# Kernel optimization log

Hardware: AMD Instinct MI355X
Metric: run time of the kernel (lower is better)

The kernel has to match this reference:

```python
import jax, jax.numpy as jnp
import numpy as np

ALPHA = 1.0  # config.cnet_alpha


def setup_inputs() -> dict:
    key = jax.random.key(0)
    k1, k2 = jax.random.split(key)
    z = jax.random.normal(k1, (8192, 2048), dtype=jnp.float32)
    centroids = jax.random.normal(k2, (512, 2048), dtype=jnp.float32)
    return {"z": z, "centroids": centroids}


def reference(z, centroids):
    # --- compute_similarity, 'EUC' branch ---
    # torch: sqrt(sum((z[None] - centroids[:, None])**2, dim=2)).T
    # computed here via the expanded quadratic form (same math, no
    # (n_clusters, bs, n_hidden) materialization):
    z_sq = jnp.sum(z * z, axis=1, keepdims=True)              # (bs, 1)
    c_sq = jnp.sum(centroids * centroids, axis=1)[None, :]    # (1, n_clusters)
    cross = jnp.einsum('bh,ch->bc', z, centroids)             # (bs, n_clusters)
    d2 = jnp.maximum(z_sq + c_sq - 2.0 * cross, 0.0)
    similarity = jnp.sqrt(d2)                                 # (bs, n_clusters)

    # --- Student-t soft assignment Q ---
    Q = jnp.power(1.0 + similarity / ALPHA, -(ALPHA + 1.0) / 2.0)
    Q = Q / jnp.nansum(Q, axis=1, keepdims=True)

    # --- target distribution P ---
    P = (Q * Q) / jnp.sum(Q, axis=0, keepdims=True)
    P = P / jnp.nansum(P, axis=1, keepdims=True)

    return jnp.stack([Q, P])  # (2, bs, n_clusters)
```

## Files before the change

### kernel.cpp

```cpp
#include <hip/hip_runtime.h>
#include <stdint.h>

#define M_ROWS 8192
#define NCLUST 512
#define KDIM   2048

#define BM 128
#define BN 128
#define BKB 128
#define KSPLIT 2
#define NKT (KDIM / KSPLIT / BKB)

typedef __attribute__((ext_vector_type(4))) int   i32x4;
typedef __attribute__((ext_vector_type(8))) int   i32x8;
typedef __attribute__((ext_vector_type(4))) float f32x4;
typedef __attribute__((ext_vector_type(8))) unsigned short u16x8;

__device__ __forceinline__ unsigned short f2bf(float f) {
    unsigned u = __float_as_uint(f);
    u += 0x7FFFu + ((u >> 16) & 1u);
    return (unsigned short)(u >> 16);
}
__device__ __forceinline__ float bf2f(unsigned short h) {
    return __uint_as_float(((unsigned)h) << 16);
}

__device__ __forceinline__ void gload_lds16(const void* g, void* l) {
    __builtin_amdgcn_global_load_lds(
        (const __attribute__((address_space(1))) void*)g,
        (__attribute__((address_space(3))) void*)l,
        16, 0, 0);
}

__global__ __launch_bounds__(256) void k_convert(
    const float* __restrict__ z, const float* __restrict__ cent,
    unsigned char* __restrict__ zb, unsigned char* __restrict__ cb,
    float* __restrict__ zsq, float* __restrict__ csq,
    float* __restrict__ colsum)
{
    int w = threadIdx.x >> 6, lane = threadIdx.x & 63;
    int row = blockIdx.x * 4 + w;

    const float* src;
    unsigned char* dst;
    float* nrm;
    int r;
    if (row < M_ROWS) { src = z + (size_t)row * KDIM; dst = zb + (size_t)row * KDIM; nrm = zsq; r = row; }
    else              { r = row - M_ROWS; src = cent + (size_t)r * KDIM; dst = cb + (size_t)r * KDIM; nrm = csq; }

    float s = 0.f;
    #pragma unroll
    for (int it = 0; it < KDIM / 256; ++it) {
        int idx = it * 256 + lane * 4;
        float4 v = *(const float4*)(src + idx);
        s += v.x * v.x + v.y * v.y + v.z * v.z + v.w * v.w;
        int p = __builtin_amdgcn_cvt_pk_fp8_f32(v.x, v.y, 0, 0);
        p     = __builtin_amdgcn_cvt_pk_fp8_f32(v.z, v.w, p, 1);
        *(int*)(dst + idx) = p;
    }
    #pragma unroll
    for (int off = 32; off; off >>= 1) s += __shfl_down(s, off);
    if (lane == 0) nrm[r] = s;

    if (blockIdx.x == 0) {
        colsum[threadIdx.x] = 0.f;
        colsum[threadIdx.x + 256] = 0.f;
    }
}

__global__ __launch_bounds__(512) void k_gemm_part(
    const unsigned char* __restrict__ zb, const unsigned char* __restrict__ cb,
    unsigned short* __restrict__ parts)
{
    __shared__ unsigned char As[2][BM * BKB];
    __shared__ unsigned char Bs[2][BN * BKB];

    const int wgid = blockIdx.x;
    const int inner = wgid >> 3;
    const int bx  = inner & 3;
    const int bz  = (inner >> 2) & 1;
    const int by  = ((inner >> 3) << 3) | (wgid & 7);
    const int bRow = by * BM;
    const int bCol = bx * BN;
    const size_t kb0 = (size_t)bz * (KDIM / KSPLIT);

    const int tid  = threadIdx.x & 255;
    const int w    = (threadIdx.x >> 6) & 3, lane = threadIdx.x & 63;
    const int wr   = w >> 1,  wc   = w & 1;

    f32x4 acc[4][4] = {};

    const int srow = lane >> 3;
    const int scol = ((lane & 7) ^ srow) * 16;
    const unsigned char* gA = zb + (size_t)(bRow + srow) * KDIM + kb0 + scol;
    const unsigned char* gB = cb + (size_t)(bCol + srow) * KDIM + kb0 + scol;

    auto stage = [&](int buf, int kt) {
        const int kb = kt * BKB;
        #pragma unroll
        for (int j = 0; j < 4; ++j) {
            const int g = w * 4 + j;
            gload_lds16(gA + (size_t)(g * 8) * KDIM + kb, &As[buf][g * 1024]);
            gload_lds16(gB + (size_t)(g * 8) * KDIM + kb, &Bs[buf][g * 1024]);
        }
    };

    const int arowb = wr * 64 + (lane & 15);
    const int bcolb = wc * 64 + (lane & 15);
    const int s     = lane >> 4;
    const int r7    = lane & 7;
    const int sc    = 0x7F7F7F7F;

    auto compute = [&](int buf) {
        const unsigned char* A0 = &As[buf][0];
        const unsigned char* B0 = &Bs[buf][0];
        i32x8 af[4], bfr[4];
        #pragma unroll
        for (int i = 0; i < 4; ++i) {
            const int row = arowb + i * 16;
            const i32x4 lo = *(const i32x4*)&A0[row * BKB + ((2 * s) ^ r7) * 16];
            const i32x4 hi = *(const i32x4*)&A0[row * BKB + ((2 * s + 1) ^ r7) * 16];
            af[i][0] = lo[0]; af[i][1] = lo[1]; af[i][2] = lo[2]; af[i][3] = lo[3];
            af[i][4] = hi[0]; af[i][5] = hi[1]; af[i][6] = hi[2]; af[i][7] = hi[3];
        }
        #pragma unroll
        for (int j = 0; j < 4; ++j) {
            const int row = bcolb + j * 16;
            const i32x4 lo = *(const i32x4*)&B0[row * BKB + ((2 * s) ^ r7) * 16];
            const i32x4 hi = *(const i32x4*)&B0[row * BKB + ((2 * s + 1) ^ r7) * 16];
            bfr[j][0] = lo[0]; bfr[j][1] = lo[1]; bfr[j][2] = lo[2]; bfr[j][3] = lo[3];
            bfr[j][4] = hi[0]; bfr[j][5] = hi[1]; bfr[j][6] = hi[2]; bfr[j][7] = hi[3];
        }
        #pragma unroll
        for (int i = 0; i < 4; ++i)
            #pragma unroll
            for (int j = 0; j < 4; ++j)
                acc[i][j] = __builtin_amdgcn_mfma_scale_f32_16x16x128_f8f6f4(
                    af[i], bfr[j], acc[i][j], 0, 0, 0, sc, 0, sc);
    };

    stage(0, 0);
    __syncthreads();
    int buf = 0;
    for (int kt = 0; kt < NKT - 1; ++kt) {
        stage(buf ^ 1, kt + 1);
        compute(buf);
        __syncthreads();
        buf ^= 1;
    }
    compute(buf);

    unsigned short* dst = parts + (size_t)bz * M_ROWS * NCLUST;
    const int col0 = bCol + wc * 64 + (lane & 15);
    const int row0 = bRow + wr * 64 + (lane >> 4) * 4;
    #pragma unroll
    for (int j = 0; j < 4; ++j) {
        const int col = col0 + j * 16;
        #pragma unroll
        for (int i = 0; i < 4; ++i)
            #pragma unroll
            for (int r = 0; r < 4; ++r)
                dst[(size_t)(row0 + i * 16 + r) * NCLUST + col] = f2bf(acc[i][j][r]);
    }
    (void)tid;
}

__global__ __launch_bounds__(256) void k_q_norm(
    const unsigned short* __restrict__ parts,
    const float* __restrict__ zsq, const float* __restrict__ csq,
    float* __restrict__ Q, float* __restrict__ colsum)
{
    __shared__ float red[4][NCLUST];
    const int tid = threadIdx.x, w = tid >> 6, lane = tid & 63;
    const size_t PSTR = (size_t)M_ROWS * NCLUST;
    float ca[8] = {0, 0, 0, 0, 0, 0, 0, 0};
    const int rbase = blockIdx.x * 32;

    float cs[8];
    {
        float4 c0 = *(const float4*)(csq + lane * 8);
        float4 c1 = *(const float4*)(csq + lane * 8 + 4);
        cs[0] = c0.x; cs[1] = c0.y; cs[2] = c0.z; cs[3] = c0.w;
        cs[4] = c1.x; cs[5] = c1.y; cs[6] = c1.z; cs[7] = c1.w;
    }

    for (int rr = 0; rr < 8; ++rr) {
        const int row = rbase + w + rr * 4;
        const size_t off = (size_t)row * NCLUST + lane * 8;
        float x[8];
        {
            u16x8 v0 = *(const u16x8*)(parts + off);
            u16x8 v1 = *(const u16x8*)(parts + PSTR + off);
            #pragma unroll
            for (int k = 0; k < 8; ++k) x[k] = bf2f(v0[k]) + bf2f(v1[k]);
        }
        const float zr = zsq[row];
        float q[8];
        float sum = 0.f;
        #pragma unroll
        for (int k = 0; k < 8; ++k) {
            q[k] = 1.0f / (1.0f + sqrtf(fmaxf(zr + cs[k] - 2.0f * x[k], 0.0f)));
            sum += q[k];
        }
        #pragma unroll
        for (int o = 32; o; o >>= 1) sum += __shfl_down(sum, o);
        sum = __shfl(sum, 0);
        const float inv = 1.0f / sum;
        float4 q0, q1;
        q0.x = q[0] * inv; q0.y = q[1] * inv; q0.z = q[2] * inv; q0.w = q[3] * inv;
        q1.x = q[4] * inv; q1.y = q[5] * inv; q1.z = q[6] * inv; q1.w = q[7] * inv;
        *(float4*)(Q + off)     = q0;
        *(float4*)(Q + off + 4) = q1;
        ca[0] += q0.x; ca[1] += q0.y; ca[2] += q0.z; ca[3] += q0.w;
        ca[4] += q1.x; ca[5] += q1.y; ca[6] += q1.z; ca[7] += q1.w;
    }
    #pragma unroll
    for (int c = 0; c < 8; ++c) red[w][lane * 8 + c] = ca[c];
    __syncthreads();
    const float t0 = red[0][tid] + red[1][tid] + red[2][tid] + red[3][tid];
    const float t1 = red[0][tid + 256] + red[1][tid + 256] + red[2][tid + 256] + red[3][tid + 256];
    atomicAdd(&colsum[tid], t0);
    atomicAdd(&colsum[tid + 256], t1);
}

__global__ __launch_bounds__(256) void k_p(
    const float* __restrict__ Q, const float* __restrict__ colsum,
    float* __restrict__ P)
{
    const int w = threadIdx.x >> 6, lane = threadIdx.x & 63;
    const int row = blockIdx.x * 4 + w;
    const float* qp = Q + (size_t)row * NCLUST;
    float4 q0 = *(const float4*)(qp + lane * 4);
    float4 q1 = *(const float4*)(qp + 256 + lane * 4);
    float4 c0 = *(const float4*)(colsum + lane * 4);
    float4 c1 = *(const float4*)(colsum + 256 + lane * 4);
    float4 p0, p1;
    p0.x = q0.x * q0.x / c0.x; p0.y = q0.y * q0.y / c0.y;
    p0.z = q0.z * q0.z / c0.z; p0.w = q0.w * q0.w / c0.w;
    p1.x = q1.x * q1.x / c1.x; p1.y = q1.y * q1.y / c1.y;
    p1.z = q1.z * q1.z / c1.z; p1.w = q1.w * q1.w / c1.w;
    float s = p0.x + p0.y + p0.z + p0.w + p1.x + p1.y + p1.z + p1.w;
    #pragma unroll
    for (int off = 32; off; off >>= 1) s += __shfl_down(s, off);
    s = __shfl(s, 0);
    const float inv = 1.0f / s;
    p0.x *= inv; p0.y *= inv; p0.z *= inv; p0.w *= inv;
    p1.x *= inv; p1.y *= inv; p1.z *= inv; p1.w *= inv;
    float* op = P + (size_t)row * NCLUST;
    *(float4*)(op + lane * 4) = p0;
    *(float4*)(op + 256 + lane * 4) = p1;
}

extern "C" void kernel_launch(void* const* d_in, const int* in_sizes, int n_in,
                              void* d_out, int out_size, void* d_ws, size_t ws_size,
                              hipStream_t stream) {
    const float* z    = (const float*)d_in[0];
    const float* cent = (const float*)d_in[1];
    float* out = (float*)d_out;

    char* ws = (char*)d_ws;
    unsigned char* zb = (unsigned char*)ws;
    unsigned char* cb = (unsigned char*)(ws + 16777216);
    float* zsq    = (float*)(ws + 17825792);
    float* csq    = (float*)(ws + 17858560);
    float* colsum = (float*)(ws + 17860608);
    unsigned short* parts = (unsigned short*)(ws + 18874368);

    float* Q = out;
    float* P = out + (size_t)M_ROWS * NCLUST;

    k_convert<<<dim3((M_ROWS + NCLUST) / 4), dim3(256), 0, stream>>>(
        z, cent, zb, cb, zsq, csq, colsum);

    k_gemm_part<<<dim3(512), dim3(256), 0, stream>>>(zb, cb, parts);

    k_q_norm<<<dim3(M_ROWS / 32), dim3(256), 0, stream>>>(
        parts, zsq, csq, Q, colsum);

    k_p<<<dim3(M_ROWS / 4), dim3(256), 0, stream>>>(Q, colsum, P);
}
```

Before: 55.93 us.

## Fuse Q and P stages into one cooperative kernel with grid sync

Replaces the separate Q-normalization and P kernels with one cooperative kernel. Each block keeps its Q rows in registers, adds its column sums atomically, waits at a grid-wide barrier, then computes P from the register copy. This avoids re-reading Q from global memory and removes one kernel launch. In exchange it relies on 512 blocks being co-resident for the cooperative launch, with a fallback to the old two-kernel path if that launch fails. The GEMM launch bounds are also corrected to 256 threads.

```diff
diff --git a/kernel.cpp b/kernel.cpp
--- a/kernel.cpp
+++ b/kernel.cpp
@@ -1,5 +1,8 @@
 #include <hip/hip_runtime.h>
+#include <hip/hip_cooperative_groups.h>
 #include <stdint.h>
+
+namespace cg = cooperative_groups;
 
 #define M_ROWS 8192
 #define NCLUST 512
@@ -68,7 +71,7 @@
     }
 }
 
-__global__ __launch_bounds__(512) void k_gemm_part(
+__global__ __launch_bounds__(256) void k_gemm_part(
     const unsigned char* __restrict__ zb, const unsigned char* __restrict__ cb,
     unsigned short* __restrict__ parts)
 {
@@ -84,8 +87,7 @@
     const int bCol = bx * BN;
     const size_t kb0 = (size_t)bz * (KDIM / KSPLIT);
 
-    const int tid  = threadIdx.x & 255;
-    const int w    = (threadIdx.x >> 6) & 3, lane = threadIdx.x & 63;
+    const int w    = threadIdx.x >> 6, lane = threadIdx.x & 63;
     const int wr   = w >> 1,  wc   = w & 1;
 
     f32x4 acc[4][4] = {};
@@ -162,7 +164,106 @@
             for (int r = 0; r < 4; ++r)
                 dst[(size_t)(row0 + i * 16 + r) * NCLUST + col] = f2bf(acc[i][j][r]);
     }
-    (void)tid;
+}
+
+__global__ __launch_bounds__(256) void k_qp_fused(
+    const unsigned short* __restrict__ parts,
+    const float* __restrict__ zsq, const float* __restrict__ csq,
+    float* __restrict__ Q, float* __restrict__ P,
+    float* __restrict__ colsum)
+{
+    cg::grid_group grid = cg::this_grid();
+    __shared__ float red[4][NCLUST];
+    __shared__ float cls[NCLUST];
+
+    const int tid = threadIdx.x, w = tid >> 6, lane = tid & 63;
+    const size_t PSTR = (size_t)M_ROWS * NCLUST;
+    const int rbase = blockIdx.x * 16;
+
+    float cs8[8];
+    {
+        float4 c0 = *(const float4*)(csq + lane * 8);
+        float4 c1 = *(const float4*)(csq + lane * 8 + 4);
+        cs8[0] = c0.x; cs8[1] = c0.y; cs8[2] = c0.z; cs8[3] = c0.w;
+        cs8[4] = c1.x; cs8[5] = c1.y; cs8[6] = c1.z; cs8[7] = c1.w;
+    }
+
+    float q[4][8];
+    float ca[8] = {0, 0, 0, 0, 0, 0, 0, 0};
+
+    #pragma unroll
+    for (int rr = 0; rr < 4; ++rr) {
+        const int row = rbase + w + rr * 4;
+        const size_t off = (size_t)row * NCLUST + lane * 8;
+        float x[8];
+        {
+            u16x8 v0 = *(const u16x8*)(parts + off);
+            u16x8 v1 = *(const u16x8*)(parts + PSTR + off);
+            #pragma unroll
+            for (int k = 0; k < 8; ++k) x[k] = bf2f(v0[k]) + bf2f(v1[k]);
+        }
+        const float zr = zsq[row];
+        float sum = 0.f;
+        #pragma unroll
+        for (int k = 0; k < 8; ++k) {
+            q[rr][k] = 1.0f / (1.0f + sqrtf(fmaxf(zr + cs8[k] - 2.0f * x[k], 0.0f)));
+            sum += q[rr][k];
+        }
+        #pragma unroll
+        for (int o = 32; o; o >>= 1) sum += __shfl_down(sum, o);
+        sum = __shfl(sum, 0);
+        const float inv = 1.0f / sum;
+        float4 q0, q1;
+        #pragma unroll
+        for (int k = 0; k < 8; ++k) q[rr][k] *= inv;
+        q0.x = q[rr][0]; q0.y = q[rr][1]; q0.z = q[rr][2]; q0.w = q[rr][3];
+        q1.x = q[rr][4]; q1.y = q[rr][5]; q1.z = q[rr][6]; q1.w = q[rr][7];
+        *(float4*)(Q + off)     = q0;
+        *(float4*)(Q + off + 4) = q1;
+        #pragma unroll
+        for (int k = 0; k < 8; ++k) ca[k] += q[rr][k];
+    }
+    #pragma unroll
+    for (int c = 0; c < 8; ++c) red[w][lane * 8 + c] = ca[c];
+    __syncthreads();
+    {
+        const float t0 = red[0][tid] + red[1][tid] + red[2][tid] + red[3][tid];
+        const float t1 = red[0][tid + 256] + red[1][tid + 256] + red[2][tid + 256] + red[3][tid + 256];
+        atomicAdd(&colsum[tid], t0);
+        atomicAdd(&colsum[tid + 256], t1);
+    }
+    __threadfence();
+    grid.sync();
+
+    cls[tid]       = __hip_atomic_load(&colsum[tid],       __ATOMIC_RELAXED, __HIP_MEMORY_SCOPE_AGENT);
+    cls[tid + 256] = __hip_atomic_load(&colsum[tid + 256], __ATOMIC_RELAXED, __HIP_MEMORY_SCOPE_AGENT);
+    __syncthreads();
+
+    float ci8[8];
+    #pragma unroll
+    for (int k = 0; k < 8; ++k) ci8[k] = 1.0f / cls[lane * 8 + k];
+
+    #pragma unroll
+    for (int rr = 0; rr < 4; ++rr) {
+        const int row = rbase + w + rr * 4;
+        float p[8];
+        float sum = 0.f;
+        #pragma unroll
+        for (int k = 0; k < 8; ++k) {
+            p[k] = q[rr][k] * q[rr][k] * ci8[k];
+            sum += p[k];
+        }
+        #pragma unroll
+        for (int o = 32; o; o >>= 1) sum += __shfl_down(sum, o);
+        sum = __shfl(sum, 0);
+        const float inv = 1.0f / sum;
+        float4 p0, p1;
+        p0.x = p[0] * inv; p0.y = p[1] * inv; p0.z = p[2] * inv; p0.w = p[3] * inv;
+        p1.x = p[4] * inv; p1.y = p[5] * inv; p1.z = p[6] * inv; p1.w = p[7] * inv;
+        const size_t off = (size_t)row * NCLUST + lane * 8;
+        *(float4*)(P + off)     = p0;
+        *(float4*)(P + off + 4) = p1;
+    }
 }
 
 __global__ __launch_bounds__(256) void k_q_norm(
@@ -274,8 +375,20 @@
 
     k_gemm_part<<<dim3(512), dim3(256), 0, stream>>>(zb, cb, parts);
 
-    k_q_norm<<<dim3(M_ROWS / 32), dim3(256), 0, stream>>>(
-        parts, zsq, csq, Q, colsum);
-
-    k_p<<<dim3(M_ROWS / 4), dim3(256), 0, stream>>>(Q, colsum, P);
-}
+    {
+        const unsigned short* parts_ = parts;
+        const float* zsq_ = zsq; const float* csq_ = csq;
+        float* Q_ = Q; float* P_ = P; float* colsum_ = colsum;
+        void* args[] = { (void*)&parts_, (void*)&zsq_, (void*)&csq_,
+                         (void*)&Q_, (void*)&P_, (void*)&colsum_ };
+        hipError_t err = hipLaunchCooperativeKernel(
+            (const void*)k_qp_fused, dim3(M_ROWS / 16), dim3(256),
+            args, 0, stream);
+        if (err != hipSuccess) {
+            (void)hipGetLastError();
+            k_q_norm<<<dim3(M_ROWS / 32), dim3(256), 0, stream>>>(
+                parts, zsq, csq, Q, colsum);
+            k_p<<<dim3(M_ROWS / 4), dim3(256), 0, stream>>>(Q, colsum, P);
+        }
+    }
+}
```

Measured after the change: 164.2 us. 194% more time.
